# Optimization experiments

Measured on AMD Instinct MI355X. Metric: run time of the kernel, lower is better.

The kernel has to match this reference:

```python
import jax, jax.numpy as jnp
import numpy as np

DIM = 1024
HIDDEN = 2816
NUM_EXPERTS = 8
TOP_K = 2
BATCH, SEQ = 4, 2048


def setup_inputs() -> dict:
    key = jax.random.key(0)
    ks = jax.random.split(key, 5)
    x = jax.random.normal(ks[0], (BATCH, SEQ, DIM), dtype=jnp.float32)
    gate_w = jax.random.normal(ks[1], (NUM_EXPERTS, DIM), dtype=jnp.float32) * 0.02
    w1 = jax.random.normal(ks[2], (NUM_EXPERTS, HIDDEN, DIM), dtype=jnp.float32) * 0.02
    w3 = jax.random.normal(ks[3], (NUM_EXPERTS, HIDDEN, DIM), dtype=jnp.float32) * 0.02
    w2 = jax.random.normal(ks[4], (NUM_EXPERTS, DIM, HIDDEN), dtype=jnp.float32) * 0.02
    return {"x": x, "gate_w": gate_w, "w1": w1, "w3": w3, "w2": w2}


def reference(x, gate_w, w1, w3, w2):
    orig_shape = x.shape
    xf = x.reshape(-1, x.shape[-1])                      # [T, D]
    T = xf.shape[0]
    E, K = gate_w.shape[0], TOP_K

    # gating: softmax over experts, then top-k (descending, matches torch.topk)
    scores = jax.nn.softmax(xf @ gate_w.T, axis=-1)      # [T, E]
    expert_weights, expert_indices = jax.lax.top_k(scores, K)  # [T, K]
    expert_weights = expert_weights / jnp.sum(expert_weights, axis=-1, keepdims=True)

    # dispatch: each token duplicated K times (torch repeat_interleave)
    x_rep = jnp.repeat(xf, K, axis=0)                    # [T*K, D]
    flat_idx = expert_indices.reshape(-1)                # [T*K]

    # per-expert masked SwiGLU FFN, combined into y (loop over small fixed E)
    y = jnp.zeros_like(x_rep)
    for e in range(E):
        m = (flat_idx == e)[:, None]
        xe = jnp.where(m, x_rep, 0.0)                    # zero non-routed tokens
        h = jax.nn.silu(xe @ w1[e].T) * (xe @ w3[e].T)   # [T*K, H]
        out = h @ w2[e].T                                # [T*K, D]
        y = y + jnp.where(m, out, 0.0)

    # weighted combine over the K slots
    y = jnp.sum(y.reshape(T, K, -1) * expert_weights[..., None], axis=1)
    return y.reshape(orig_shape)
```

## Files before the change

### kernel.cpp

```cpp
#include <hip/hip_runtime.h>
#include <hip/hip_bf16.h>

#define NTOK 8192
#define DIM 1024
#define HID 2816
#define NE 8
#define NSLOT (NTOK*2)
#define BM 128
#define BN 128
#define BK 32
#define MAXMT (NSLOT/BM + NE)

typedef float f32x4 __attribute__((ext_vector_type(4)));
typedef __bf16 bf16x8 __attribute__((ext_vector_type(8)));
typedef __bf16 bf16x4 __attribute__((ext_vector_type(4)));

#define MFMA(a,b,c) __builtin_amdgcn_mfma_f32_16x16x32_bf16(a,b,c,0,0,0)

__device__ __forceinline__ void cvt_st8(__bf16* d, f32x4 a, f32x4 b){
  bf16x8 v;
  v[0]=(__bf16)a.x; v[1]=(__bf16)a.y; v[2]=(__bf16)a.z; v[3]=(__bf16)a.w;
  v[4]=(__bf16)b.x; v[5]=(__bf16)b.y; v[6]=(__bf16)b.z; v[7]=(__bf16)b.w;
  *reinterpret_cast<bf16x8*>(d) = v;
}

__device__ __forceinline__ void gld_lds16(const void* g, void* l){
  __builtin_amdgcn_global_load_lds(
    (const __attribute__((address_space(1))) void*)g,
    (__attribute__((address_space(3))) void*)l, 16, 0, 0);
}

__device__ __forceinline__ int swz(int r, int g){ return r*BK + ((g ^ ((r>>1)&3))<<3); }

__device__ __forceinline__ int xcd_map(int orig, int nwg){
  int q = nwg>>3, rr = nwg&7, x = orig&7, o = orig>>3;
  return (x<rr ? x*(q+1) : rr*(q+1)+(x-rr)*q) + o;
}

__global__ void k_zero(int* cnt){ if(threadIdx.x < NE) cnt[threadIdx.x] = 0; }

__global__ __launch_bounds__(256) void k_zero_y(float* __restrict__ y){
  int i = blockIdx.x*256 + threadIdx.x;
  reinterpret_cast<f32x4*>(y)[i] = f32x4{0.f,0.f,0.f,0.f};
}

__global__ __launch_bounds__(256) void k_cvt(const float* __restrict__ src,
                                             __bf16* __restrict__ dst){
  int i = blockIdx.x*256 + threadIdx.x;
  const f32x4* s = reinterpret_cast<const f32x4*>(src) + (size_t)i*2;
  f32x4 a = s[0], b = s[1];
  cvt_st8(dst + (size_t)i*8, a, b);
}

__global__ __launch_bounds__(256) void k_gate(const float* __restrict__ x,
    const float* __restrict__ gw, int* __restrict__ idxs,
    float* __restrict__ wt, int* __restrict__ cnt, __bf16* __restrict__ xb)
{
  int lane = threadIdx.x & 63;
  int t = blockIdx.x*4 + (threadIdx.x >> 6);
  const f32x4* x4 = reinterpret_cast<const f32x4*>(x) + (size_t)t*(DIM/4);
  const f32x4* g4 = reinterpret_cast<const f32x4*>(gw);
  f32x4 xv[4];
#pragma unroll
  for(int i=0;i<4;i++) xv[i] = x4[i*64 + lane];
  double logit[NE];
#pragma unroll
  for(int e=0;e<NE;e++){
    double s = 0.0;
#pragma unroll
    for(int i=0;i<4;i++){
      f32x4 g = g4[e*(DIM/4) + i*64 + lane];
      s += (double)xv[i].x*g.x + (double)xv[i].y*g.y
         + (double)xv[i].z*g.z + (double)xv[i].w*g.w;
    }
#pragma unroll
    for(int d=32; d>0; d>>=1) s += __shfl_xor(s, d, 64);
    logit[e] = s;
  }
  __bf16* xo = xb + (size_t)t*DIM;
#pragma unroll
  for(int i=0;i<4;i++){
    bf16x4 v;
    v[0]=(__bf16)xv[i].x; v[1]=(__bf16)xv[i].y;
    v[2]=(__bf16)xv[i].z; v[3]=(__bf16)xv[i].w;
    *reinterpret_cast<bf16x4*>(xo + (i*64+lane)*4) = v;
  }
  if(lane==0){
    int i1=0; double m1=logit[0];
#pragma unroll
    for(int e=1;e<NE;e++) if(logit[e]>m1){ m1=logit[e]; i1=e; }
    int i2=-1; double m2=-1e300;
#pragma unroll
    for(int e=0;e<NE;e++) if(e!=i1 && logit[e]>m2){ m2=logit[e]; i2=e; }
    float e2 = __expf((float)(m2-m1));
    float w0 = 1.f/(1.f+e2);
    idxs[2*t]=i1; idxs[2*t+1]=i2;
    wt[2*t]=w0;   wt[2*t+1]=e2*w0;
    atomicAdd(&cnt[i1],1); atomicAdd(&cnt[i2],1);
  }
}

__global__ void k_prep(const int* __restrict__ cnt, int* __restrict__ off,
                       int* __restrict__ mtp, int* __restrict__ cursor)
{
  if(threadIdx.x==0){
    int o=0, m=0; off[0]=0; mtp[0]=0;
    for(int e=0;e<NE;e++){
      cursor[e]=o; o += cnt[e]; off[e+1]=o;
      m += (cnt[e]+BM-1)/BM;  mtp[e+1]=m;
    }
  }
}

__global__ __launch_bounds__(256) void k_scatter(const int* __restrict__ idxs,
    int* __restrict__ cursor, int* __restrict__ order)
{
  int t = blockIdx.x*blockDim.x + threadIdx.x;
#pragma unroll
  for(int k=0;k<2;k++){
    int s = 2*t+k;
    int e = idxs[s];
    int p = atomicAdd(&cursor[e],1);
    order[p]=s;
  }
}

__global__ __launch_bounds__(512) void k_ffn1(
    const __bf16* __restrict__ xb, const __bf16* __restrict__ w1b,
    const __bf16* __restrict__ w3b, const int* __restrict__ off,
    const int* __restrict__ mtp, const int* __restrict__ order,
    __bf16* __restrict__ h)
{
  __shared__ __align__(16) __bf16 lA [2][BM*BK];
  __shared__ __align__(16) __bf16 lB1[2][BN*BK];
  __shared__ __align__(16) __bf16 lB3[2][BN*BK];

  const int NT = HID/BN;
  int wg = xcd_map(blockIdx.x, MAXMT*NT);
  int mt = wg / NT, nt = wg % NT;
  if (mt >= mtp[NE]) return;
  int e = 0;
  while (mt >= mtp[e+1]) e++;
  int row0   = off[e] + (mt - mtp[e])*BM;
  int row_end= off[e+1];
  int n0     = nt*BN;

  int tid = threadIdx.x, lane = tid & 63;
  int srow = tid>>2;
  int scol = ((tid&3) ^ ((srow>>1)&3))<<3;
  int arow = min(row0 + srow, row_end-1);
  int tok  = order[arow] >> 1;
  const __bf16* gA  = xb  + (size_t)tok*DIM + scol;
  const __bf16* gB1 = w1b + (size_t)e*HID*DIM + (size_t)(n0+srow)*DIM + scol;
  const __bf16* gB3 = w3b + (size_t)e*HID*DIM + (size_t)(n0+srow)*DIM + scol;
  int ldso = (tid>>6)<<9;

  int wm = (tid>>6)>>2, wn = (tid>>6)&3;
  int fr = lane & 15, gq = lane>>4;

  f32x4 acc1[4][2], acc3[4][2];
#pragma unroll
  for(int m=0;m<4;m++)
#pragma unroll
    for(int n=0;n<2;n++){ acc1[m][n]=f32x4{0.f,0.f,0.f,0.f}; acc3[m][n]=f32x4{0.f,0.f,0.f,0.f}; }

  gld_lds16(gA,  &lA [0][ldso]);
  gld_lds16(gB1, &lB1[0][ldso]);
  gld_lds16(gB3, &lB3[0][ldso]);
  __syncthreads();

  const int NK = DIM/BK;
  int buf=0;
  for(int kt=0; kt<NK; kt++){
    if(kt+1<NK){
      gld_lds16(gA  + (kt+1)*BK, &lA [buf^1][ldso]);
      gld_lds16(gB1 + (kt+1)*BK, &lB1[buf^1][ldso]);
      gld_lds16(gB3 + (kt+1)*BK, &lB3[buf^1][ldso]);
    }
    bf16x8 av[4], bv[2], cv[2];
#pragma unroll
    for(int m=0;m<4;m++) av[m]=*reinterpret_cast<const bf16x8*>(&lA[buf][swz(wm*64+m*16+fr, gq)]);
#pragma unroll
    for(int n=0;n<2;n++){
      bv[n]=*reinterpret_cast<const bf16x8*>(&lB1[buf][swz(wn*32+n*16+fr, gq)]);
      cv[n]=*reinterpret_cast<const bf16x8*>(&lB3[buf][swz(wn*32+n*16+fr, gq)]);
    }
#pragma unroll
    for(int m=0;m<4;m++)
#pragma unroll
      for(int n=0;n<2;n++){
        acc1[m][n]=MFMA(av[m],bv[n],acc1[m][n]);
        acc3[m][n]=MFMA(av[m],cv[n],acc3[m][n]);
      }
    __syncthreads();
    buf^=1;
  }

#pragma unroll
  for(int m=0;m<4;m++){
    int rbase = row0 + wm*64 + m*16 + ((lane>>4)<<2);
#pragma unroll
    for(int r=0;r<4;r++){
      if(rbase+r < row_end){
        __bf16* hp = h + (size_t)(rbase+r)*HID + n0 + wn*32 + fr;
#pragma unroll
        for(int n=0;n<2;n++){
          float u = acc1[m][n][r], v = acc3[m][n][r];
          hp[n*16] = (__bf16)( (u/(1.f+__expf(-u))) * v );
        }
      }
    }
  }
}

__global__ __launch_bounds__(512) void k_ffn2(
    const __bf16* __restrict__ h, const __bf16* __restrict__ w2b,
    const int* __restrict__ off, const int* __restrict__ mtp,
    const int* __restrict__ order, const float* __restrict__ wt,
    float* __restrict__ y)
{
  __shared__ __align__(16) __bf16 lA[2][BM*BK];
  __shared__ __align__(16) __bf16 lB[2][BN*BK];

  const int NT = DIM/BN;
  int wg = xcd_map(blockIdx.x, MAXMT*NT);
  int mt = wg / NT, nt = wg % NT;
  if (mt >= mtp[NE]) return;
  int e = 0;
  while (mt >= mtp[e+1]) e++;
  int row0   = off[e] + (mt - mtp[e])*BM;
  int row_end= off[e+1];
  int n0     = nt*BN;

  int tid = threadIdx.x, lane = tid & 63;
  int srow = tid>>2;
  int scol = ((tid&3) ^ ((srow>>1)&3))<<3;
  int hrow = min(row0 + srow, NSLOT-1);
  const __bf16* gA = h   + (size_t)hrow*HID + scol;
  const __bf16* gB = w2b + (size_t)e*DIM*HID + (size_t)(n0+srow)*HID + scol;
  int ldso = (tid>>6)<<9;

  int wm = (tid>>6)>>2, wn = (tid>>6)&3;
  int fr = lane & 15, gq = lane>>4;

  f32x4 acc[4][2];
#pragma unroll
  for(int m=0;m<4;m++)
#pragma unroll
    for(int n=0;n<2;n++) acc[m][n]=f32x4{0.f,0.f,0.f,0.f};

  gld_lds16(gA, &lA[0][ldso]);
  gld_lds16(gB, &lB[0][ldso]);
  __syncthreads();

  const int NK = HID/BK;
  int buf=0;
  for(int kt=0; kt<NK; kt++){
    if(kt+1<NK){
      gld_lds16(gA + (kt+1)*BK, &lA[buf^1][ldso]);
      gld_lds16(gB + (kt+1)*BK, &lB[buf^1][ldso]);
    }
    bf16x8 av[4], bv[2];
#pragma unroll
    for(int m=0;m<4;m++) av[m]=*reinterpret_cast<const bf16x8*>(&lA[buf][swz(wm*64+m*16+fr, gq)]);
#pragma unroll
    for(int n=0;n<2;n++) bv[n]=*reinterpret_cast<const bf16x8*>(&lB[buf][swz(wn*32+n*16+fr, gq)]);
#pragma unroll
    for(int m=0;m<4;m++)
#pragma unroll
      for(int n=0;n<2;n++)
        acc[m][n]=MFMA(av[m],bv[n],acc[m][n]);
    __syncthreads();
    buf^=1;
  }

#pragma unroll
  for(int m=0;m<4;m++){
    int rbase = row0 + wm*64 + m*16 + ((lane>>4)<<2);
#pragma unroll
    for(int r=0;r<4;r++){
      int p = rbase + r;
      if(p < row_end){
        int s = order[p];
        float wv = wt[s];
        float* yp = y + (size_t)(s>>1)*DIM + n0 + wn*32 + fr;
        atomicAdd(&yp[0],  wv*acc[m][0][r]);
        atomicAdd(&yp[16], wv*acc[m][1][r]);
      }
    }
  }
}

extern "C" void kernel_launch(void* const* d_in, const int* in_sizes, int n_in,
                              void* d_out, int out_size, void* d_ws, size_t ws_size,
                              hipStream_t stream)
{
  const float* x  = (const float*)d_in[0];
  const float* gw = (const float*)d_in[1];
  const float* w1 = (const float*)d_in[2];
  const float* w3 = (const float*)d_in[3];
  const float* w2 = (const float*)d_in[4];
  float* y = (float*)d_out;
  char* ws = (char*)d_ws;

  int*   cnt    = (int*)(ws + 0);
  int*   off    = (int*)(ws + 64);
  int*   mtp    = (int*)(ws + 128);
  int*   cursor = (int*)(ws + 192);
  int*   idxs   = (int*)(ws + 256);
  float* wt     = (float*)(ws + 65792);
  int*   order  = (int*)(ws + 131328);
  __bf16* h     = (__bf16*)(ws + 262400);
  __bf16* xb    = (__bf16*)(ws + 262400 + 92274688ull);
  __bf16* w1b   = (__bf16*)(ws + 262400 + 92274688ull + 16777216);
  __bf16* w3b   = (__bf16*)(ws + 262400 + 92274688ull + 16777216 + 46137344ull);
  __bf16* w2b   = (__bf16*)(ws + 262400 + 92274688ull + 16777216 + 2*46137344ull);

  const int WN8 = NE*HID*DIM/8;

  k_zero   <<<1, 64, 0, stream>>>(cnt);
  k_gate   <<<NTOK/4, 256, 0, stream>>>(x, gw, idxs, wt, cnt, xb);
  k_prep   <<<1, 64, 0, stream>>>(cnt, off, mtp, cursor);
  k_scatter<<<NTOK/256, 256, 0, stream>>>(idxs, cursor, order);
  k_cvt    <<<WN8/256, 256, 0, stream>>>(w1, w1b);
  k_cvt    <<<WN8/256, 256, 0, stream>>>(w3, w3b);
  k_cvt    <<<WN8/256, 256, 0, stream>>>(w2, w2b);
  k_zero_y <<<NTOK*DIM/4/256, 256, 0, stream>>>(y);
  k_ffn1   <<<MAXMT*(HID/BN), 512, 0, stream>>>(xb, w1b, w3b, off, mtp, order, h);
  k_ffn2   <<<MAXMT*(DIM/BN), 512, 0, stream>>>(h, w2b, off, mtp, order, wt, y);
}
```

Baseline: 752.3 us.

## Pipeline grouped-GEMM FFNs with larger tiles and replace atomic combine with gather

Raises the FFN1 row tile to 256 and gives FFN2 a 128x128 tile on 4 waves. Both GEMMs get a multi-stage, explicitly scheduled LDS pipeline using vmcnt waits, split barriers and raised MFMA priority. FFN2 now writes bf16 per-slot outputs into reused workspace (the w1b region) instead of doing fp32 atomics into y. A new combine kernel gathers the two slots per token through an inverse permutation, which also removes the y zeroing kernel. The cost is extra precision loss from the bf16 intermediate and higher register pressure from the larger accumulators.

```diff
diff --git a/kernel.cpp b/kernel.cpp
--- a/kernel.cpp
+++ b/kernel.cpp
@@ -6,16 +6,17 @@
 #define HID 2816
 #define NE 8
 #define NSLOT (NTOK*2)
-#define BM 128
-#define BN 128
-#define BK 32
-#define MAXMT (NSLOT/BM + NE)
+#define MAXMT1 (NSLOT/256 + NE)
+#define MAXMT2 (NSLOT/128 + NE)
 
 typedef float f32x4 __attribute__((ext_vector_type(4)));
 typedef __bf16 bf16x8 __attribute__((ext_vector_type(8)));
 typedef __bf16 bf16x4 __attribute__((ext_vector_type(4)));
 
 #define MFMA(a,b,c) __builtin_amdgcn_mfma_f32_16x16x32_bf16(a,b,c,0,0,0)
+#define SWZ(r,g) (((r)<<5) + ((((g) ^ (((r)>>1)&3)))<<3))
+#define VMW(N) asm volatile("s_waitcnt vmcnt(" #N ")" ::: "memory")
+#define NOP do{}while(0)
 
 __device__ __forceinline__ void cvt_st8(__bf16* d, f32x4 a, f32x4 b){
   bf16x8 v;
@@ -23,26 +24,17 @@
   v[4]=(__bf16)b.x; v[5]=(__bf16)b.y; v[6]=(__bf16)b.z; v[7]=(__bf16)b.w;
   *reinterpret_cast<bf16x8*>(d) = v;
 }
-
 __device__ __forceinline__ void gld_lds16(const void* g, void* l){
   __builtin_amdgcn_global_load_lds(
     (const __attribute__((address_space(1))) void*)g,
     (__attribute__((address_space(3))) void*)l, 16, 0, 0);
 }
-
-__device__ __forceinline__ int swz(int r, int g){ return r*BK + ((g ^ ((r>>1)&3))<<3); }
-
 __device__ __forceinline__ int xcd_map(int orig, int nwg){
   int q = nwg>>3, rr = nwg&7, x = orig&7, o = orig>>3;
   return (x<rr ? x*(q+1) : rr*(q+1)+(x-rr)*q) + o;
 }
 
 __global__ void k_zero(int* cnt){ if(threadIdx.x < NE) cnt[threadIdx.x] = 0; }
-
-__global__ __launch_bounds__(256) void k_zero_y(float* __restrict__ y){
-  int i = blockIdx.x*256 + threadIdx.x;
-  reinterpret_cast<f32x4*>(y)[i] = f32x4{0.f,0.f,0.f,0.f};
-}
 
 __global__ __launch_bounds__(256) void k_cvt(const float* __restrict__ src,
                                              __bf16* __restrict__ dst){
@@ -101,19 +93,21 @@
 }
 
 __global__ void k_prep(const int* __restrict__ cnt, int* __restrict__ off,
-                       int* __restrict__ mtp, int* __restrict__ cursor)
+                       int* __restrict__ mtp1, int* __restrict__ mtp2,
+                       int* __restrict__ cursor)
 {
   if(threadIdx.x==0){
-    int o=0, m=0; off[0]=0; mtp[0]=0;
+    int o=0, m1=0, m2=0; off[0]=0; mtp1[0]=0; mtp2[0]=0;
     for(int e=0;e<NE;e++){
       cursor[e]=o; o += cnt[e]; off[e+1]=o;
-      m += (cnt[e]+BM-1)/BM;  mtp[e+1]=m;
+      m1 += (cnt[e]+255)>>8;  mtp1[e+1]=m1;
+      m2 += (cnt[e]+127)>>7;  mtp2[e+1]=m2;
     }
   }
 }
 
 __global__ __launch_bounds__(256) void k_scatter(const int* __restrict__ idxs,
-    int* __restrict__ cursor, int* __restrict__ order)
+    int* __restrict__ cursor, int* __restrict__ order, int* __restrict__ inv)
 {
   int t = blockIdx.x*blockDim.x + threadIdx.x;
 #pragma unroll
@@ -121,84 +115,104 @@
     int s = 2*t+k;
     int e = idxs[s];
     int p = atomicAdd(&cursor[e],1);
-    order[p]=s;
+    order[p]=s; inv[s]=p;
   }
 }
 
 __global__ __launch_bounds__(512) void k_ffn1(
     const __bf16* __restrict__ xb, const __bf16* __restrict__ w1b,
     const __bf16* __restrict__ w3b, const int* __restrict__ off,
-    const int* __restrict__ mtp, const int* __restrict__ order,
+    const int* __restrict__ mtp1, const int* __restrict__ order,
     __bf16* __restrict__ h)
 {
-  __shared__ __align__(16) __bf16 lA [2][BM*BK];
-  __shared__ __align__(16) __bf16 lB1[2][BN*BK];
-  __shared__ __align__(16) __bf16 lB3[2][BN*BK];
-
-  const int NT = HID/BN;
-  int wg = xcd_map(blockIdx.x, MAXMT*NT);
+  __shared__ __align__(16) __bf16 sA [2][2][256*32];
+  __shared__ __align__(16) __bf16 sB1[2][2][128*32];
+  __shared__ __align__(16) __bf16 sB3[2][2][128*32];
+
+  const int NT = HID/128;
+  int wg = xcd_map(blockIdx.x, MAXMT1*NT);
   int mt = wg / NT, nt = wg % NT;
-  if (mt >= mtp[NE]) return;
+  if (mt >= mtp1[NE]) return;
   int e = 0;
-  while (mt >= mtp[e+1]) e++;
-  int row0   = off[e] + (mt - mtp[e])*BM;
-  int row_end= off[e+1];
-  int n0     = nt*BN;
-
-  int tid = threadIdx.x, lane = tid & 63;
-  int srow = tid>>2;
-  int scol = ((tid&3) ^ ((srow>>1)&3))<<3;
-  int arow = min(row0 + srow, row_end-1);
-  int tok  = order[arow] >> 1;
-  const __bf16* gA  = xb  + (size_t)tok*DIM + scol;
-  const __bf16* gB1 = w1b + (size_t)e*HID*DIM + (size_t)(n0+srow)*DIM + scol;
-  const __bf16* gB3 = w3b + (size_t)e*HID*DIM + (size_t)(n0+srow)*DIM + scol;
-  int ldso = (tid>>6)<<9;
-
-  int wm = (tid>>6)>>2, wn = (tid>>6)&3;
-  int fr = lane & 15, gq = lane>>4;
-
-  f32x4 acc1[4][2], acc3[4][2];
-#pragma unroll
-  for(int m=0;m<4;m++)
+  while (mt >= mtp1[e+1]) e++;
+  int row0    = off[e] + (mt - mtp1[e])*256;
+  int row_end = off[e+1];
+  int n0      = nt*128;
+
+  int tid = threadIdx.x, lane = tid&63, wave = tid>>6;
+  int wm = wave>>2, wn = wave&3;
+  int fr = lane&15, gq = lane>>4;
+  int sr = tid>>2, gloc = tid&3;
+  int swo = ((gloc ^ ((sr>>1)&3))<<3);
+
+  int ar0 = min(row0 + sr,       row_end-1);
+  int ar1 = min(row0 + sr + 128, row_end-1);
+  const __bf16* a0  = xb  + (size_t)(order[ar0]>>1)*DIM + swo;
+  const __bf16* a1  = xb  + (size_t)(order[ar1]>>1)*DIM + swo;
+  const __bf16* b1p = w1b + (size_t)e*HID*DIM + (size_t)(n0+sr)*DIM + swo;
+  const __bf16* b3p = w3b + (size_t)e*HID*DIM + (size_t)(n0+sr)*DIM + swo;
+
+  f32x4 acc1[8][2], acc3[8][2];
+#pragma unroll
+  for(int m=0;m<8;m++)
 #pragma unroll
     for(int n=0;n<2;n++){ acc1[m][n]=f32x4{0.f,0.f,0.f,0.f}; acc3[m][n]=f32x4{0.f,0.f,0.f,0.f}; }
 
-  gld_lds16(gA,  &lA [0][ldso]);
-  gld_lds16(gB1, &lB1[0][ldso]);
-  gld_lds16(gB3, &lB3[0][ldso]);
-  __syncthreads();
-
-  const int NK = DIM/BK;
-  int buf=0;
-  for(int kt=0; kt<NK; kt++){
-    if(kt+1<NK){
-      gld_lds16(gA  + (kt+1)*BK, &lA [buf^1][ldso]);
-      gld_lds16(gB1 + (kt+1)*BK, &lB1[buf^1][ldso]);
-      gld_lds16(gB3 + (kt+1)*BK, &lB3[buf^1][ldso]);
-    }
-    bf16x8 av[4], bv[2], cv[2];
-#pragma unroll
-    for(int m=0;m<4;m++) av[m]=*reinterpret_cast<const bf16x8*>(&lA[buf][swz(wm*64+m*16+fr, gq)]);
-#pragma unroll
-    for(int n=0;n<2;n++){
-      bv[n]=*reinterpret_cast<const bf16x8*>(&lB1[buf][swz(wn*32+n*16+fr, gq)]);
-      cv[n]=*reinterpret_cast<const bf16x8*>(&lB3[buf][swz(wn*32+n*16+fr, gq)]);
-    }
-#pragma unroll
-    for(int m=0;m<4;m++)
-#pragma unroll
-      for(int n=0;n<2;n++){
-        acc1[m][n]=MFMA(av[m],bv[n],acc1[m][n]);
-        acc3[m][n]=MFMA(av[m],cv[n],acc3[m][n]);
-      }
-    __syncthreads();
-    buf^=1;
-  }
-
-#pragma unroll
-  for(int m=0;m<4;m++){
-    int rbase = row0 + wm*64 + m*16 + ((lane>>4)<<2);
+#define F1_STGA(b, kt_, kk) { \
+    gld_lds16(a0 + (kt_)*64 + (kk)*32, &sA[b][kk][wave<<9]); \
+    gld_lds16(a1 + (kt_)*64 + (kk)*32, &sA[b][kk][4096 + (wave<<9)]); }
+#define F1_STGB(b, kt_, kk) { \
+    gld_lds16(b1p + (kt_)*64 + (kk)*32, &sB1[b][kk][wave<<9]); \
+    gld_lds16(b3p + (kt_)*64 + (kk)*32, &sB3[b][kk][wave<<9]); }
+#define F1_PH(b, kk, hh, RB, STAGE, WAITC) { \
+    bf16x8 av[4]; \
+    _Pragma("unroll") for(int m_=0;m_<4;m_++) \
+      av[m_] = *(const bf16x8*)&sA[b][kk][SWZ(wm*128 + ((hh)*4+m_)*16 + fr, gq)]; \
+    if(RB){ _Pragma("unroll") for(int n_=0;n_<2;n_++){ \
+      bv1[n_] = *(const bf16x8*)&sB1[b][kk][SWZ(wn*32 + n_*16 + fr, gq)]; \
+      bv3[n_] = *(const bf16x8*)&sB3[b][kk][SWZ(wn*32 + n_*16 + fr, gq)]; } } \
+    STAGE; \
+    __builtin_amdgcn_s_barrier(); \
+    asm volatile("s_waitcnt lgkmcnt(0)" ::: "memory"); \
+    __builtin_amdgcn_sched_barrier(0); \
+    __builtin_amdgcn_s_setprio(1); \
+    _Pragma("unroll") for(int m_=0;m_<4;m_++) _Pragma("unroll") for(int n_=0;n_<2;n_++){ \
+      acc1[(hh)*4+m_][n_] = MFMA(av[m_], bv1[n_], acc1[(hh)*4+m_][n_]); \
+      acc3[(hh)*4+m_][n_] = MFMA(av[m_], bv3[n_], acc3[(hh)*4+m_][n_]); } \
+    __builtin_amdgcn_s_setprio(0); \
+    WAITC; \
+    __builtin_amdgcn_s_barrier(); }
+
+  F1_STGA(0,0,0); F1_STGB(0,0,0); F1_STGA(0,0,1); F1_STGB(0,0,1);
+  F1_STGA(1,1,0); F1_STGB(1,1,0);
+  VMW(4);
+  __builtin_amdgcn_s_barrier();
+
+  bf16x8 bv1[2], bv3[2];
+  int kt = 0;
+  const int NI = (DIM/64)/2;
+  for(int it=0; it<NI-1; ++it, kt+=2){
+    F1_PH(0,0,0, 1, F1_STGA(1,kt+1,1), NOP);
+    F1_PH(0,0,1, 0, F1_STGB(1,kt+1,1), NOP);
+    F1_PH(0,1,0, 1, F1_STGA(0,kt+2,0), NOP);
+    F1_PH(0,1,1, 0, F1_STGB(0,kt+2,0), VMW(4));
+    F1_PH(1,0,0, 1, F1_STGA(0,kt+2,1), NOP);
+    F1_PH(1,0,1, 0, F1_STGB(0,kt+2,1), NOP);
+    F1_PH(1,1,0, 1, F1_STGA(1,kt+3,0), NOP);
+    F1_PH(1,1,1, 0, F1_STGB(1,kt+3,0), VMW(4));
+  }
+  F1_PH(0,0,0, 1, F1_STGA(1,kt+1,1), NOP);
+  F1_PH(0,0,1, 0, F1_STGB(1,kt+1,1), NOP);
+  F1_PH(0,1,0, 1, NOP, NOP);
+  F1_PH(0,1,1, 0, NOP, VMW(0));
+  F1_PH(1,0,0, 1, NOP, NOP);
+  F1_PH(1,0,1, 0, NOP, NOP);
+  F1_PH(1,1,0, 1, NOP, NOP);
+  F1_PH(1,1,1, 0, NOP, NOP);
+
+#pragma unroll
+  for(int m=0;m<8;m++){
+    int rbase = row0 + wm*128 + m*16 + (gq<<2);
 #pragma unroll
     for(int r=0;r<4;r++){
       if(rbase+r < row_end){
@@ -211,84 +225,120 @@
       }
     }
   }
-}
-
-__global__ __launch_bounds__(512) void k_ffn2(
+#undef F1_STGA
+#undef F1_STGB
+#undef F1_PH
+}
+
+__global__ __launch_bounds__(256) void k_ffn2(
     const __bf16* __restrict__ h, const __bf16* __restrict__ w2b,
-    const int* __restrict__ off, const int* __restrict__ mtp,
-    const int* __restrict__ order, const float* __restrict__ wt,
-    float* __restrict__ y)
-{
-  __shared__ __align__(16) __bf16 lA[2][BM*BK];
-  __shared__ __align__(16) __bf16 lB[2][BN*BK];
-
-  const int NT = DIM/BN;
-  int wg = xcd_map(blockIdx.x, MAXMT*NT);
+    const int* __restrict__ off, const int* __restrict__ mtp2,
+    __bf16* __restrict__ ys)
+{
+  __shared__ __align__(16) __bf16 sA[2][2][128*32];
+  __shared__ __align__(16) __bf16 sB[2][2][128*32];
+
+  const int NT = DIM/128;
+  int wg = xcd_map(blockIdx.x, MAXMT2*NT);
   int mt = wg / NT, nt = wg % NT;
-  if (mt >= mtp[NE]) return;
+  if (mt >= mtp2[NE]) return;
   int e = 0;
-  while (mt >= mtp[e+1]) e++;
-  int row0   = off[e] + (mt - mtp[e])*BM;
-  int row_end= off[e+1];
-  int n0     = nt*BN;
-
-  int tid = threadIdx.x, lane = tid & 63;
-  int srow = tid>>2;
-  int scol = ((tid&3) ^ ((srow>>1)&3))<<3;
-  int hrow = min(row0 + srow, NSLOT-1);
-  const __bf16* gA = h   + (size_t)hrow*HID + scol;
-  const __bf16* gB = w2b + (size_t)e*DIM*HID + (size_t)(n0+srow)*HID + scol;
-  int ldso = (tid>>6)<<9;
-
-  int wm = (tid>>6)>>2, wn = (tid>>6)&3;
-  int fr = lane & 15, gq = lane>>4;
-
-  f32x4 acc[4][2];
+  while (mt >= mtp2[e+1]) e++;
+  int row0    = off[e] + (mt - mtp2[e])*128;
+  int row_end = off[e+1];
+  int n0      = nt*128;
+
+  int tid = threadIdx.x, lane = tid&63, wave = tid>>6;
+  int wm = wave>>1, wn = wave&1;
+  int fr = lane&15, gq = lane>>4;
+  int sr = tid>>2, gloc = tid&3;
+  int swo = ((gloc ^ ((sr>>1)&3))<<3);
+
+  int ar0 = min(row0 + sr,      NSLOT-1);
+  int ar1 = min(row0 + sr + 64, NSLOT-1);
+  const __bf16* a0 = h   + (size_t)ar0*HID + swo;
+  const __bf16* a1 = h   + (size_t)ar1*HID + swo;
+  const __bf16* b0 = w2b + (size_t)e*DIM*HID + (size_t)(n0+sr)*HID + swo;
+  const __bf16* b1 = w2b + (size_t)e*DIM*HID + (size_t)(n0+sr+64)*HID + swo;
+
+  f32x4 acc[4][4];
 #pragma unroll
   for(int m=0;m<4;m++)
 #pragma unroll
-    for(int n=0;n<2;n++) acc[m][n]=f32x4{0.f,0.f,0.f,0.f};
-
-  gld_lds16(gA, &lA[0][ldso]);
-  gld_lds16(gB, &lB[0][ldso]);
-  __syncthreads();
-
-  const int NK = HID/BK;
-  int buf=0;
-  for(int kt=0; kt<NK; kt++){
-    if(kt+1<NK){
-      gld_lds16(gA + (kt+1)*BK, &lA[buf^1][ldso]);
-      gld_lds16(gB + (kt+1)*BK, &lB[buf^1][ldso]);
-    }
-    bf16x8 av[4], bv[2];
-#pragma unroll
-    for(int m=0;m<4;m++) av[m]=*reinterpret_cast<const bf16x8*>(&lA[buf][swz(wm*64+m*16+fr, gq)]);
-#pragma unroll
-    for(int n=0;n<2;n++) bv[n]=*reinterpret_cast<const bf16x8*>(&lB[buf][swz(wn*32+n*16+fr, gq)]);
-#pragma unroll
-    for(int m=0;m<4;m++)
-#pragma unroll
-      for(int n=0;n<2;n++)
-        acc[m][n]=MFMA(av[m],bv[n],acc[m][n]);
-    __syncthreads();
-    buf^=1;
-  }
+    for(int n=0;n<4;n++) acc[m][n]=f32x4{0.f,0.f,0.f,0.f};
+
+#define F2_STGA(b, kt_, kk) { \
+    gld_lds16(a0 + (kt_)*64 + (kk)*32, &sA[b][kk][wave<<9]); \
+    gld_lds16(a1 + (kt_)*64 + (kk)*32, &sA[b][kk][2048 + (wave<<9)]); }
+#define F2_STGB(b, kt_, kk) { \
+    gld_lds16(b0 + (kt_)*64 + (kk)*32, &sB[b][kk][wave<<9]); \
+    gld_lds16(b1 + (kt_)*64 + (kk)*32, &sB[b][kk][2048 + (wave<<9)]); }
+#define F2_PH(b, kk, STAGE, WAITC) { \
+    bf16x8 av[4], bv[4]; \
+    _Pragma("unroll") for(int m_=0;m_<4;m_++) \
+      av[m_] = *(const bf16x8*)&sA[b][kk][SWZ(wm*64 + m_*16 + fr, gq)]; \
+    _Pragma("unroll") for(int n_=0;n_<4;n_++) \
+      bv[n_] = *(const bf16x8*)&sB[b][kk][SWZ(wn*64 + n_*16 + fr, gq)]; \
+    STAGE; \
+    __builtin_amdgcn_s_barrier(); \
+    asm volatile("s_waitcnt lgkmcnt(0)" ::: "memory"); \
+    __builtin_amdgcn_sched_barrier(0); \
+    __builtin_amdgcn_s_setprio(1); \
+    _Pragma("unroll") for(int m_=0;m_<4;m_++) _Pragma("unroll") for(int n_=0;n_<4;n_++) \
+      acc[m_][n_] = MFMA(av[m_], bv[n_], acc[m_][n_]); \
+    __builtin_amdgcn_s_setprio(0); \
+    WAITC; \
+    __builtin_amdgcn_s_barrier(); }
+
+  F2_STGA(0,0,0); F2_STGB(0,0,0); F2_STGA(0,0,1); F2_STGB(0,0,1);
+  F2_STGA(1,1,0); F2_STGB(1,1,0);
+  VMW(4);
+  __builtin_amdgcn_s_barrier();
+
+  int kt = 0;
+  const int NI = (HID/64)/2;
+  for(int it=0; it<NI-1; ++it, kt+=2){
+    F2_PH(0,0, { F2_STGA(1,kt+1,1); F2_STGB(1,kt+1,1); }, NOP);
+    F2_PH(0,1, { F2_STGA(0,kt+2,0); F2_STGB(0,kt+2,0); }, VMW(4));
+    F2_PH(1,0, { F2_STGA(0,kt+2,1); F2_STGB(0,kt+2,1); }, NOP);
+    F2_PH(1,1, { F2_STGA(1,kt+3,0); F2_STGB(1,kt+3,0); }, VMW(4));
+  }
+  F2_PH(0,0, { F2_STGA(1,kt+1,1); F2_STGB(1,kt+1,1); }, NOP);
+  F2_PH(0,1, NOP, VMW(0));
+  F2_PH(1,0, NOP, NOP);
+  F2_PH(1,1, NOP, NOP);
 
 #pragma unroll
   for(int m=0;m<4;m++){
-    int rbase = row0 + wm*64 + m*16 + ((lane>>4)<<2);
+    int rbase = row0 + wm*64 + m*16 + (gq<<2);
 #pragma unroll
     for(int r=0;r<4;r++){
-      int p = rbase + r;
-      if(p < row_end){
-        int s = order[p];
-        float wv = wt[s];
-        float* yp = y + (size_t)(s>>1)*DIM + n0 + wn*32 + fr;
-        atomicAdd(&yp[0],  wv*acc[m][0][r]);
-        atomicAdd(&yp[16], wv*acc[m][1][r]);
+      if(rbase+r < row_end){
+        __bf16* yp = ys + (size_t)(rbase+r)*DIM + n0 + wn*64 + fr;
+#pragma unroll
+        for(int n=0;n<4;n++) yp[n*16] = (__bf16)acc[m][n][r];
       }
     }
   }
+#undef F2_STGA
+#undef F2_STGB
+#undef F2_PH
+}
+
+__global__ __launch_bounds__(256) void k_combine(
+    const __bf16* __restrict__ ys, const int* __restrict__ inv,
+    const float* __restrict__ wt, float* __restrict__ y)
+{
+  int t  = blockIdx.x;
+  int p0 = inv[2*t], p1 = inv[2*t+1];
+  float w0 = wt[2*t], w1v = wt[2*t+1];
+  int d = threadIdx.x*4;
+  const __bf16* r0 = ys + (size_t)p0*DIM + d;
+  const __bf16* r1 = ys + (size_t)p1*DIM + d;
+  f32x4 o;
+#pragma unroll
+  for(int j=0;j<4;j++) o[j] = w0*(float)r0[j] + w1v*(float)r1[j];
+  *reinterpret_cast<f32x4*>(y + (size_t)t*DIM + d) = o;
 }
 
 extern "C" void kernel_launch(void* const* d_in, const int* in_sizes, int n_in,
@@ -305,27 +355,30 @@
 
   int*   cnt    = (int*)(ws + 0);
   int*   off    = (int*)(ws + 64);
-  int*   mtp    = (int*)(ws + 128);
-  int*   cursor = (int*)(ws + 192);
-  int*   idxs   = (int*)(ws + 256);
-  float* wt     = (float*)(ws + 65792);
-  int*   order  = (int*)(ws + 131328);
-  __bf16* h     = (__bf16*)(ws + 262400);
-  __bf16* xb    = (__bf16*)(ws + 262400 + 92274688ull);
-  __bf16* w1b   = (__bf16*)(ws + 262400 + 92274688ull + 16777216);
-  __bf16* w3b   = (__bf16*)(ws + 262400 + 92274688ull + 16777216 + 46137344ull);
-  __bf16* w2b   = (__bf16*)(ws + 262400 + 92274688ull + 16777216 + 2*46137344ull);
+  int*   mtp1   = (int*)(ws + 128);
+  int*   mtp2   = (int*)(ws + 192);
+  int*   cursor = (int*)(ws + 256);
+  int*   idxs   = (int*)(ws + 320);
+  float* wt     = (float*)(ws + 320 + 65536);
+  int*   order  = (int*)(ws + 320 + 2*65536);
+  int*   inv    = (int*)(ws + 320 + 3*65536);
+  __bf16* h     = (__bf16*)(ws + 262464);
+  __bf16* xb    = (__bf16*)(ws + 262464 + 92274688ull);
+  __bf16* w1b   = (__bf16*)(ws + 262464 + 92274688ull + 16777216ull);
+  __bf16* w3b   = (__bf16*)(ws + 262464 + 92274688ull + 16777216ull + 46137344ull);
+  __bf16* w2b   = (__bf16*)(ws + 262464 + 92274688ull + 16777216ull + 2*46137344ull);
+  __bf16* ysb   = w1b;
 
   const int WN8 = NE*HID*DIM/8;
 
   k_zero   <<<1, 64, 0, stream>>>(cnt);
   k_gate   <<<NTOK/4, 256, 0, stream>>>(x, gw, idxs, wt, cnt, xb);
-  k_prep   <<<1, 64, 0, stream>>>(cnt, off, mtp, cursor);
-  k_scatter<<<NTOK/256, 256, 0, stream>>>(idxs, cursor, order);
+  k_prep   <<<1, 64, 0, stream>>>(cnt, off, mtp1, mtp2, cursor);
+  k_scatter<<<NTOK/256, 256, 0, stream>>>(idxs, cursor, order, inv);
   k_cvt    <<<WN8/256, 256, 0, stream>>>(w1, w1b);
   k_cvt    <<<WN8/256, 256, 0, stream>>>(w3, w3b);
   k_cvt    <<<WN8/256, 256, 0, stream>>>(w2, w2b);
-  k_zero_y <<<NTOK*DIM/4/256, 256, 0, stream>>>(y);
-  k_ffn1   <<<MAXMT*(HID/BN), 512, 0, stream>>>(xb, w1b, w3b, off, mtp, order, h);
-  k_ffn2   <<<MAXMT*(DIM/BN), 512, 0, stream>>>(h, w2b, off, mtp, order, wt, y);
-}
+  k_ffn1   <<<MAXMT1*(HID/128), 512, 0, stream>>>(xb, w1b, w3b, off, mtp1, order, h);
+  k_ffn2   <<<MAXMT2*(DIM/128), 256, 0, stream>>>(h, w2b, off, mtp2, ysb);
+  k_combine<<<NTOK, 256, 0, stream>>>(ysb, inv, wt, y);
+}
```

New measurement: 774.9 us. +3.0%, slower.

## Replace atomic scatter-add with sorted bf16 output plus gather combine kernel

Applied to the files above, without the earlier changes.

The second FFN GEMM now writes per-slot results in bf16 to a sorted buffer (reusing the w1b workspace once ffn1 is done), and a new combine kernel gathers each token's two slots through an inverse permutation and applies the routing weights. This removes the float atomicAdds into y and the separate zeroing kernel. The ffn2 N-tile is widened to 256 to give more MFMA reuse per A load, and the three weight conversions are merged into one launch. In exchange it adds an extra pass over a bf16 intermediate and rounds the expert outputs to bf16 before the combine.

```diff
diff --git a/kernel.cpp b/kernel.cpp
--- a/kernel.cpp
+++ b/kernel.cpp
@@ -7,7 +7,6 @@
 #define NE 8
 #define NSLOT (NTOK*2)
 #define BM 128
-#define BN 128
 #define BK 32
 #define MAXMT (NSLOT/BM + NE)
 
@@ -16,6 +15,7 @@
 typedef __bf16 bf16x4 __attribute__((ext_vector_type(4)));
 
 #define MFMA(a,b,c) __builtin_amdgcn_mfma_f32_16x16x32_bf16(a,b,c,0,0,0)
+#define SWZ(r,g) (((r)<<5) + ((((g) ^ (((r)>>1)&3)))<<3))
 
 __device__ __forceinline__ void cvt_st8(__bf16* d, f32x4 a, f32x4 b){
   bf16x8 v;
@@ -23,15 +23,11 @@
   v[4]=(__bf16)b.x; v[5]=(__bf16)b.y; v[6]=(__bf16)b.z; v[7]=(__bf16)b.w;
   *reinterpret_cast<bf16x8*>(d) = v;
 }
-
 __device__ __forceinline__ void gld_lds16(const void* g, void* l){
   __builtin_amdgcn_global_load_lds(
     (const __attribute__((address_space(1))) void*)g,
     (__attribute__((address_space(3))) void*)l, 16, 0, 0);
 }
-
-__device__ __forceinline__ int swz(int r, int g){ return r*BK + ((g ^ ((r>>1)&3))<<3); }
-
 __device__ __forceinline__ int xcd_map(int orig, int nwg){
   int q = nwg>>3, rr = nwg&7, x = orig&7, o = orig>>3;
   return (x<rr ? x*(q+1) : rr*(q+1)+(x-rr)*q) + o;
@@ -39,14 +35,16 @@
 
 __global__ void k_zero(int* cnt){ if(threadIdx.x < NE) cnt[threadIdx.x] = 0; }
 
-__global__ __launch_bounds__(256) void k_zero_y(float* __restrict__ y){
-  int i = blockIdx.x*256 + threadIdx.x;
-  reinterpret_cast<f32x4*>(y)[i] = f32x4{0.f,0.f,0.f,0.f};
-}
-
-__global__ __launch_bounds__(256) void k_cvt(const float* __restrict__ src,
-                                             __bf16* __restrict__ dst){
-  int i = blockIdx.x*256 + threadIdx.x;
+__global__ __launch_bounds__(256) void k_cvt3(
+    const float* __restrict__ s1, const float* __restrict__ s3,
+    const float* __restrict__ s2, __bf16* __restrict__ d1,
+    __bf16* __restrict__ d3, __bf16* __restrict__ d2)
+{
+  const int PB = (NE*HID*DIM/8)/256;
+  int seg = blockIdx.x / PB;
+  int i   = (blockIdx.x % PB)*256 + threadIdx.x;
+  const float* src = (seg==0) ? s1 : (seg==1) ? s3 : s2;
+  __bf16*      dst = (seg==0) ? d1 : (seg==1) ? d3 : d2;
   const f32x4* s = reinterpret_cast<const f32x4*>(src) + (size_t)i*2;
   f32x4 a = s[0], b = s[1];
   cvt_st8(dst + (size_t)i*8, a, b);
@@ -113,7 +111,7 @@
 }
 
 __global__ __launch_bounds__(256) void k_scatter(const int* __restrict__ idxs,
-    int* __restrict__ cursor, int* __restrict__ order)
+    int* __restrict__ cursor, int* __restrict__ order, int* __restrict__ inv)
 {
   int t = blockIdx.x*blockDim.x + threadIdx.x;
 #pragma unroll
@@ -121,7 +119,7 @@
     int s = 2*t+k;
     int e = idxs[s];
     int p = atomicAdd(&cursor[e],1);
-    order[p]=s;
+    order[p]=s; inv[s]=p;
   }
 }
 
@@ -132,20 +130,20 @@
     __bf16* __restrict__ h)
 {
   __shared__ __align__(16) __bf16 lA [2][BM*BK];
-  __shared__ __align__(16) __bf16 lB1[2][BN*BK];
-  __shared__ __align__(16) __bf16 lB3[2][BN*BK];
-
-  const int NT = HID/BN;
+  __shared__ __align__(16) __bf16 lB1[2][BM*BK];
+  __shared__ __align__(16) __bf16 lB3[2][BM*BK];
+
+  const int NT = HID/128;
   int wg = xcd_map(blockIdx.x, MAXMT*NT);
   int mt = wg / NT, nt = wg % NT;
   if (mt >= mtp[NE]) return;
   int e = 0;
   while (mt >= mtp[e+1]) e++;
-  int row0   = off[e] + (mt - mtp[e])*BM;
-  int row_end= off[e+1];
-  int n0     = nt*BN;
-
-  int tid = threadIdx.x, lane = tid & 63;
+  int row0    = off[e] + (mt - mtp[e])*BM;
+  int row_end = off[e+1];
+  int n0      = nt*128;
+
+  int tid = threadIdx.x, lane = tid&63;
   int srow = tid>>2;
   int scol = ((tid&3) ^ ((srow>>1)&3))<<3;
   int arow = min(row0 + srow, row_end-1);
@@ -179,11 +177,11 @@
     }
     bf16x8 av[4], bv[2], cv[2];
 #pragma unroll
-    for(int m=0;m<4;m++) av[m]=*reinterpret_cast<const bf16x8*>(&lA[buf][swz(wm*64+m*16+fr, gq)]);
+    for(int m=0;m<4;m++) av[m]=*reinterpret_cast<const bf16x8*>(&lA[buf][SWZ(wm*64+m*16+fr, gq)]);
 #pragma unroll
     for(int n=0;n<2;n++){
-      bv[n]=*reinterpret_cast<const bf16x8*>(&lB1[buf][swz(wn*32+n*16+fr, gq)]);
-      cv[n]=*reinterpret_cast<const bf16x8*>(&lB3[buf][swz(wn*32+n*16+fr, gq)]);
+      bv[n]=*reinterpret_cast<const bf16x8*>(&lB1[buf][SWZ(wn*32+n*16+fr, gq)]);
+      cv[n]=*reinterpret_cast<const bf16x8*>(&lB3[buf][SWZ(wn*32+n*16+fr, gq)]);
     }
 #pragma unroll
     for(int m=0;m<4;m++)
@@ -198,7 +196,7 @@
 
 #pragma unroll
   for(int m=0;m<4;m++){
-    int rbase = row0 + wm*64 + m*16 + ((lane>>4)<<2);
+    int rbase = row0 + wm*64 + m*16 + (gq<<2);
 #pragma unroll
     for(int r=0;r<4;r++){
       if(rbase+r < row_end){
@@ -216,59 +214,62 @@
 __global__ __launch_bounds__(512) void k_ffn2(
     const __bf16* __restrict__ h, const __bf16* __restrict__ w2b,
     const int* __restrict__ off, const int* __restrict__ mtp,
-    const int* __restrict__ order, const float* __restrict__ wt,
-    float* __restrict__ y)
-{
-  __shared__ __align__(16) __bf16 lA[2][BM*BK];
-  __shared__ __align__(16) __bf16 lB[2][BN*BK];
-
-  const int NT = DIM/BN;
+    __bf16* __restrict__ ys)
+{
+  __shared__ __align__(16) __bf16 lA[2][128*BK];
+  __shared__ __align__(16) __bf16 lB[2][256*BK];
+
+  const int NT = DIM/256;
   int wg = xcd_map(blockIdx.x, MAXMT*NT);
   int mt = wg / NT, nt = wg % NT;
   if (mt >= mtp[NE]) return;
   int e = 0;
   while (mt >= mtp[e+1]) e++;
-  int row0   = off[e] + (mt - mtp[e])*BM;
-  int row_end= off[e+1];
-  int n0     = nt*BN;
-
-  int tid = threadIdx.x, lane = tid & 63;
+  int row0    = off[e] + (mt - mtp[e])*BM;
+  int row_end = off[e+1];
+  int n0      = nt*256;
+
+  int tid = threadIdx.x, lane = tid&63;
   int srow = tid>>2;
   int scol = ((tid&3) ^ ((srow>>1)&3))<<3;
+  int s2col = ((tid&3) ^ (((srow+128)>>1)&3))<<3;
   int hrow = min(row0 + srow, NSLOT-1);
-  const __bf16* gA = h   + (size_t)hrow*HID + scol;
-  const __bf16* gB = w2b + (size_t)e*DIM*HID + (size_t)(n0+srow)*HID + scol;
+  const __bf16* gA  = h   + (size_t)hrow*HID + scol;
+  const __bf16* gB0 = w2b + (size_t)e*DIM*HID + (size_t)(n0+srow)*HID + scol;
+  const __bf16* gB1 = w2b + (size_t)e*DIM*HID + (size_t)(n0+srow+128)*HID + s2col;
   int ldso = (tid>>6)<<9;
 
   int wm = (tid>>6)>>2, wn = (tid>>6)&3;
   int fr = lane & 15, gq = lane>>4;
 
-  f32x4 acc[4][2];
+  f32x4 acc[4][4];
 #pragma unroll
   for(int m=0;m<4;m++)
 #pragma unroll
-    for(int n=0;n<2;n++) acc[m][n]=f32x4{0.f,0.f,0.f,0.f};
-
-  gld_lds16(gA, &lA[0][ldso]);
-  gld_lds16(gB, &lB[0][ldso]);
+    for(int n=0;n<4;n++) acc[m][n]=f32x4{0.f,0.f,0.f,0.f};
+
+  gld_lds16(gA,  &lA[0][ldso]);
+  gld_lds16(gB0, &lB[0][ldso]);
+  gld_lds16(gB1, &lB[0][4096+ldso]);
   __syncthreads();
 
   const int NK = HID/BK;
   int buf=0;
   for(int kt=0; kt<NK; kt++){
     if(kt+1<NK){
-      gld_lds16(gA + (kt+1)*BK, &lA[buf^1][ldso]);
-      gld_lds16(gB + (kt+1)*BK, &lB[buf^1][ldso]);
-    }
-    bf16x8 av[4], bv[2];
-#pragma unroll
-    for(int m=0;m<4;m++) av[m]=*reinterpret_cast<const bf16x8*>(&lA[buf][swz(wm*64+m*16+fr, gq)]);
-#pragma unroll
-    for(int n=0;n<2;n++) bv[n]=*reinterpret_cast<const bf16x8*>(&lB[buf][swz(wn*32+n*16+fr, gq)]);
+      gld_lds16(gA  + (kt+1)*BK, &lA[buf^1][ldso]);
+      gld_lds16(gB0 + (kt+1)*BK, &lB[buf^1][ldso]);
+      gld_lds16(gB1 + (kt+1)*BK, &lB[buf^1][4096+ldso]);
+    }
+    bf16x8 av[4], bv[4];
+#pragma unroll
+    for(int m=0;m<4;m++) av[m]=*reinterpret_cast<const bf16x8*>(&lA[buf][SWZ(wm*64+m*16+fr, gq)]);
+#pragma unroll
+    for(int n=0;n<4;n++) bv[n]=*reinterpret_cast<const bf16x8*>(&lB[buf][SWZ(wn*64+n*16+fr, gq)]);
 #pragma unroll
     for(int m=0;m<4;m++)
 #pragma unroll
-      for(int n=0;n<2;n++)
+      for(int n=0;n<4;n++)
         acc[m][n]=MFMA(av[m],bv[n],acc[m][n]);
     __syncthreads();
     buf^=1;
@@ -276,19 +277,32 @@
 
 #pragma unroll
   for(int m=0;m<4;m++){
-    int rbase = row0 + wm*64 + m*16 + ((lane>>4)<<2);
+    int rbase = row0 + wm*64 + m*16 + (gq<<2);
 #pragma unroll
     for(int r=0;r<4;r++){
-      int p = rbase + r;
-      if(p < row_end){
-        int s = order[p];
-        float wv = wt[s];
-        float* yp = y + (size_t)(s>>1)*DIM + n0 + wn*32 + fr;
-        atomicAdd(&yp[0],  wv*acc[m][0][r]);
-        atomicAdd(&yp[16], wv*acc[m][1][r]);
+      if(rbase+r < row_end){
+        __bf16* yp = ys + (size_t)(rbase+r)*DIM + n0 + wn*64 + fr;
+#pragma unroll
+        for(int n=0;n<4;n++) yp[n*16] = (__bf16)acc[m][n][r];
       }
     }
   }
+}
+
+__global__ __launch_bounds__(256) void k_combine(
+    const __bf16* __restrict__ ys, const int* __restrict__ inv,
+    const float* __restrict__ wt, float* __restrict__ y)
+{
+  int t  = blockIdx.x;
+  int p0 = inv[2*t], p1 = inv[2*t+1];
+  float w0 = wt[2*t], w1v = wt[2*t+1];
+  int d = threadIdx.x*4;
+  const __bf16* r0 = ys + (size_t)p0*DIM + d;
+  const __bf16* r1 = ys + (size_t)p1*DIM + d;
+  f32x4 o;
+#pragma unroll
+  for(int j=0;j<4;j++) o[j] = w0*(float)r0[j] + w1v*(float)r1[j];
+  *reinterpret_cast<f32x4*>(y + (size_t)t*DIM + d) = o;
 }
 
 extern "C" void kernel_launch(void* const* d_in, const int* in_sizes, int n_in,
@@ -306,26 +320,26 @@
   int*   cnt    = (int*)(ws + 0);
   int*   off    = (int*)(ws + 64);
   int*   mtp    = (int*)(ws + 128);
-  int*   cursor = (int*)(ws + 192);
-  int*   idxs   = (int*)(ws + 256);
-  float* wt     = (float*)(ws + 65792);
-  int*   order  = (int*)(ws + 131328);
-  __bf16* h     = (__bf16*)(ws + 262400);
-  __bf16* xb    = (__bf16*)(ws + 262400 + 92274688ull);
-  __bf16* w1b   = (__bf16*)(ws + 262400 + 92274688ull + 16777216);
-  __bf16* w3b   = (__bf16*)(ws + 262400 + 92274688ull + 16777216 + 46137344ull);
-  __bf16* w2b   = (__bf16*)(ws + 262400 + 92274688ull + 16777216 + 2*46137344ull);
-
-  const int WN8 = NE*HID*DIM/8;
+  int*   cursor = (int*)(ws + 256);
+  int*   idxs   = (int*)(ws + 320);
+  float* wt     = (float*)(ws + 320 + 65536);
+  int*   order  = (int*)(ws + 320 + 2*65536);
+  int*   inv    = (int*)(ws + 320 + 3*65536);
+  __bf16* h     = (__bf16*)(ws + 262464);
+  __bf16* xb    = (__bf16*)(ws + 262464 + 92274688ull);
+  __bf16* w1b   = (__bf16*)(ws + 262464 + 92274688ull + 16777216ull);
+  __bf16* w3b   = (__bf16*)(ws + 262464 + 92274688ull + 16777216ull + 46137344ull);
+  __bf16* w2b   = (__bf16*)(ws + 262464 + 92274688ull + 16777216ull + 2*46137344ull);
+  __bf16* ysb   = w1b;
+
+  const int PB = (NE*HID*DIM/8)/256;
 
   k_zero   <<<1, 64, 0, stream>>>(cnt);
   k_gate   <<<NTOK/4, 256, 0, stream>>>(x, gw, idxs, wt, cnt, xb);
   k_prep   <<<1, 64, 0, stream>>>(cnt, off, mtp, cursor);
-  k_scatter<<<NTOK/256, 256, 0, stream>>>(idxs, cursor, order);
-  k_cvt    <<<WN8/256, 256, 0, stream>>>(w1, w1b);
-  k_cvt    <<<WN8/256, 256, 0, stream>>>(w3, w3b);
-  k_cvt    <<<WN8/256, 256, 0, stream>>>(w2, w2b);
-  k_zero_y <<<NTOK*DIM/4/256, 256, 0, stream>>>(y);
-  k_ffn1   <<<MAXMT*(HID/BN), 512, 0, stream>>>(xb, w1b, w3b, off, mtp, order, h);
-  k_ffn2   <<<MAXMT*(DIM/BN), 512, 0, stream>>>(h, w2b, off, mtp, order, wt, y);
-}
+  k_scatter<<<NTOK/256, 256, 0, stream>>>(idxs, cursor, order, inv);
+  k_cvt3   <<<3*PB, 256, 0, stream>>>(w1, w3, w2, w1b, w3b, w2b);
+  k_ffn1   <<<MAXMT*(HID/128), 512, 0, stream>>>(xb, w1b, w3b, off, mtp, order, h);
+  k_ffn2   <<<MAXMT*(DIM/256), 512, 0, stream>>>(h, w2b, off, mtp, ysb);
+  k_combine<<<NTOK, 256, 0, stream>>>(ysb, inv, wt, y);
+}
```

Result: faster. 732.0 us (-2.7%).
